# Kernel optimization log

Measured on AMD Instinct MI355X. Metric: run time of the kernel, lower is better.

## Reference

```python
import jax, jax.numpy as jnp
import numpy as np

N = 100000      # nodes
E = 600000      # directed edges
D_IN = 128
D_H = 128
D_OUT = 128
EPS = 1e-5      # BatchNorm eps


def setup_inputs() -> dict:
    key = jax.random.key(0)
    ks = jax.random.split(key, 6)
    x = jax.random.normal(ks[0], (N, D_IN), dtype=jnp.float32)
    edge_index = jax.random.randint(ks[1], (2, E), 0, N, dtype=jnp.int64)
    s1 = 1.0 / np.sqrt(D_IN)
    s2 = 1.0 / np.sqrt(D_H)
    W1 = jax.random.uniform(ks[2], (D_IN, D_H), minval=-s1, maxval=s1, dtype=jnp.float32)
    b1 = jnp.zeros((D_H,), jnp.float32)
    gamma1 = jnp.ones((D_H,), jnp.float32)
    beta1 = jnp.zeros((D_H,), jnp.float32)
    W2 = jax.random.uniform(ks[3], (D_H, D_OUT), minval=-s2, maxval=s2, dtype=jnp.float32)
    b2 = jnp.zeros((D_OUT,), jnp.float32)
    return dict(x=x, edge_index=edge_index, W1=W1, b1=b1,
                gamma1=gamma1, beta1=beta1, W2=W2, b2=b2)


def _gcn_conv(x, W, b, src, dst):
    # PyG GCNConv: h = D^{-1/2} (A + I) D^{-1/2} (x @ W) + b
    n = x.shape[0]
    h = x @ W                                   # [N, d_out]
    loop = jnp.arange(n, dtype=src.dtype)
    s = jnp.concatenate([src, loop])            # self loops appended
    d = jnp.concatenate([dst, loop])
    deg = jax.ops.segment_sum(jnp.ones_like(d, jnp.float32), d, num_segments=n)
    dinv = jax.lax.rsqrt(deg)                   # deg >= 1 after self loops
    norm = dinv[s] * dinv[d]                    # [E + N]
    agg = jax.ops.segment_sum(h[s] * norm[:, None], d, num_segments=n)  # [N, d_out]
    return agg + b


def reference(x, edge_index, W1, b1, gamma1, beta1, W2, b2):
    src, dst = edge_index[0], edge_index[1]
    # layer 0: GCNConv -> BatchNorm1d (training batch stats) -> ReLU (dropout p=0)
    h = _gcn_conv(x, W1, b1, src, dst)
    mean = h.mean(axis=0)
    var = h.var(axis=0)                         # biased variance, as torch BN
    h = (h - mean) * jax.lax.rsqrt(var + EPS) * gamma1 + beta1
    h = jax.nn.relu(h)
    # final layer: GCNConv only
    return _gcn_conv(h, W2, b2, src, dst)
```

## Files before the change

### kernel.cpp

```cpp
#include <hip/hip_runtime.h>

#define D 128
#define EPSV 1e-5f

typedef __attribute__((ext_vector_type(8))) short bf16x8;
typedef __attribute__((ext_vector_type(4))) float f32x4;

__device__ __forceinline__ short f2bf(float f){
  unsigned u = __float_as_uint(f);
  u += 0x7fffu + ((u >> 16) & 1u);
  return (short)(u >> 16);
}
__device__ __forceinline__ float bflo(unsigned u){ return __uint_as_float(u << 16); }
__device__ __forceinline__ float bfhi(unsigned u){ return __uint_as_float(u & 0xffff0000u); }
__device__ __forceinline__ float bf2f(short s){ return __uint_as_float(((unsigned)(unsigned short)s) << 16); }
__device__ __forceinline__ unsigned packbf(float a, float b){
  unsigned lo = (unsigned short)f2bf(a);
  unsigned hi = (unsigned short)f2bf(b);
  return lo | (hi << 16);
}

__global__ void k_init(int N, int E, const int* __restrict__ ei, int* __restrict__ flag,
                       int* __restrict__ deg, int* __restrict__ fill, float* __restrict__ gpart,
                       int* __restrict__ sflg,
                       const float* __restrict__ W1, const float* __restrict__ W2,
                       short* __restrict__ w1t, short* __restrict__ w2t){
  int i = blockIdx.x*blockDim.x + threadIdx.x;
  if (i < N){ deg[i] = 0; fill[i] = 0; }
  if (i < D*D){
    int j = i >> 7, k = i & 127;
    w1t[i] = f2bf(W1[k*D + j]);
    w2t[i] = f2bf(W2[k*D + j]);
  }
  if (i < 2048) gpart[i] = 0.f;
  if (i < 128) sflg[i] = 0;
  if (blockIdx.x == 0){
    __shared__ int any;
    int t = threadIdx.x;
    if (t == 0) any = 0;
    __syncthreads();
    if (2*t+1 < 2*E && ei[2*t+1] != 0) atomicOr(&any, 1);
    __syncthreads();
    if (t == 0) flag[0] = (any == 0) ? 1 : 0;
  }
}

__global__ void k_scan(const int* __restrict__ deg, int N, int* __restrict__ rowp,
                       float* __restrict__ dinv, int* __restrict__ s_agg,
                       int* __restrict__ s_inc, int* __restrict__ s_flg){
  __shared__ int sh[256];
  __shared__ int s_ex;
  int b = blockIdx.x, t = threadIdx.x;
  int base = b*1024 + t*4;
  int c0 = (base+0 < N) ? deg[base+0] : 0;
  int c1 = (base+1 < N) ? deg[base+1] : 0;
  int c2 = (base+2 < N) ? deg[base+2] : 0;
  int c3 = (base+3 < N) ? deg[base+3] : 0;
  int s = c0 + c1 + c2 + c3;
  sh[t] = s; __syncthreads();
  for (int d = 1; d < 256; d <<= 1){
    int v = (t >= d) ? sh[t-d] : 0;
    __syncthreads();
    sh[t] += v;
    __syncthreads();
  }
  int total = sh[255];
  if (t == 0){
    atomicExch(&s_agg[b], total);
    __threadfence();
    atomicExch(&s_flg[b], 1);
    int ex = 0;
    for (int i = b-1; i >= 0; ){
      int f;
      while ((f = atomicAdd(&s_flg[i], 0)) == 0) __builtin_amdgcn_s_sleep(1);
      if (f == 2){ ex += atomicAdd(&s_inc[i], 0); break; }
      ex += atomicAdd(&s_agg[i], 0); --i;
    }
    atomicExch(&s_inc[b], ex + total);
    __threadfence();
    atomicExch(&s_flg[b], 2);
    s_ex = ex;
  }
  __syncthreads();
  int o = sh[t] - s + s_ex;
  if (base+0 < N){ rowp[base+0] = o; dinv[base+0] = rsqrtf((float)(c0+1)); } o += c0;
  if (base+1 < N){ rowp[base+1] = o; dinv[base+1] = rsqrtf((float)(c1+1)); } o += c1;
  if (base+2 < N){ rowp[base+2] = o; dinv[base+2] = rsqrtf((float)(c2+1)); } o += c2;
  if (base+3 < N){ rowp[base+3] = o; dinv[base+3] = rsqrtf((float)(c3+1)); }
}

__global__ void k_scatter(const int* __restrict__ ei, int E, const int* __restrict__ flag,
                          const int* __restrict__ rowp, int* __restrict__ fill,
                          const float* __restrict__ dinv, int2* __restrict__ epack){
  int e = blockIdx.x*blockDim.x + threadIdx.x;
  if (e >= E) return;
  int s, d;
  if (flag[0]){ s = ei[2*e]; d = ei[2*E + 2*e]; }
  else        { s = ei[e];   d = ei[E + e];     }
  int pos = rowp[d] + atomicAdd(&fill[d], 1);
  int2 ev; ev.x = s; ev.y = __float_as_int(dinv[s] * dinv[d]);
  epack[pos] = ev;
}

template<int MODE>
__global__ __launch_bounds__(256, 2) void k_gemm(const void* __restrict__ A,
                                const short* __restrict__ BT, short* __restrict__ C, int N,
                                const float* __restrict__ gpart, const float* __restrict__ gamma,
                                const float* __restrict__ beta,
                                const int* __restrict__ ei, int E, const int* __restrict__ flag,
                                int* __restrict__ deg, int ngemmb){
  if (MODE == 1 && (int)blockIdx.x >= ngemmb){
    int cb = blockIdx.x - ngemmb;
    int e0 = cb*1024 + threadIdx.x;
    int f = flag[0];
    #pragma unroll
    for (int r = 0; r < 4; ++r){
      int e = e0 + r*256;
      if (e < E){
        int d = f ? ei[2*E + 2*e] : ei[E + e];
        atomicAdd(&deg[d], 1);
      }
    }
    return;
  }
  __shared__ short ldsB[16384];
  __shared__ short ldsC[4*2048];
  __shared__ __align__(16) float s_sc[128];
  __shared__ __align__(16) float s_sh[128];
  int w = threadIdx.x >> 6;
  int lane = threadIdx.x & 63;
  int m = lane & 15, quad = lane >> 4;

  if (MODE == 2 && threadIdx.x < 128){
    int f = threadIdx.x;
    float s = 0.f, q = 0.f;
    #pragma unroll
    for (int i = 0; i < 8; ++i){ s += gpart[i*256 + f]; q += gpart[i*256 + 128 + f]; }
    float inv = 1.f / (float)N;
    float mean = s * inv;
    float var  = q * inv - mean*mean;
    float sc = gamma[f] * rsqrtf(var + EPSV);
    s_sc[f] = sc;
    s_sh[f] = beta[f] - mean * sc;
  }
  {
    const bf16x8* BTv = (const bf16x8*)BT;
    bf16x8* Bw = (bf16x8*)ldsB;
    for (int g = threadIdx.x; g < 2048; g += 256){
      int row = g >> 4, ch = g & 15;
      Bw[row*16 + (ch ^ (row & 15))] = BTv[g];
    }
  }
  __syncthreads();
  const bf16x8* Bv = (const bf16x8*)ldsB;
  short* cw = ldsC + w*2048;

  int tiles = (N + 31) >> 5;
  int wid = blockIdx.x*4 + w;
  int wstride = ngemmb*4;
  for (int tile = wid; tile < tiles; tile += wstride){
    int r0 = tile << 5;
    bf16x8 a[2][4];
    #pragma unroll
    for (int g = 0; g < 2; ++g){
      int row = r0 + g*16 + m;
      if (row >= N) row = N - 1;
      #pragma unroll
      for (int kc = 0; kc < 4; ++kc){
        int k0 = kc*32 + quad*8;
        if (MODE == 1){
          const float* Af = (const float*)A + (size_t)row*D + k0;
          float4 u = *(const float4*)Af;
          float4 v = *(const float4*)(Af + 4);
          bf16x8 tv;
          tv[0]=f2bf(u.x); tv[1]=f2bf(u.y); tv[2]=f2bf(u.z); tv[3]=f2bf(u.w);
          tv[4]=f2bf(v.x); tv[5]=f2bf(v.y); tv[6]=f2bf(v.z); tv[7]=f2bf(v.w);
          a[g][kc] = tv;
        } else {
          bf16x8 raw = *(const bf16x8*)((const short*)A + (size_t)row*D + k0);
          float4 s0v = *(const float4*)(s_sc + k0);
          float4 s1v = *(const float4*)(s_sc + k0 + 4);
          float4 h0v = *(const float4*)(s_sh + k0);
          float4 h1v = *(const float4*)(s_sh + k0 + 4);
          bf16x8 tv;
          tv[0] = f2bf(fmaxf(fmaf(bf2f(raw[0]), s0v.x, h0v.x), 0.f));
          tv[1] = f2bf(fmaxf(fmaf(bf2f(raw[1]), s0v.y, h0v.y), 0.f));
          tv[2] = f2bf(fmaxf(fmaf(bf2f(raw[2]), s0v.z, h0v.z), 0.f));
          tv[3] = f2bf(fmaxf(fmaf(bf2f(raw[3]), s0v.w, h0v.w), 0.f));
          tv[4] = f2bf(fmaxf(fmaf(bf2f(raw[4]), s1v.x, h1v.x), 0.f));
          tv[5] = f2bf(fmaxf(fmaf(bf2f(raw[5]), s1v.y, h1v.y), 0.f));
          tv[6] = f2bf(fmaxf(fmaf(bf2f(raw[6]), s1v.z, h1v.z), 0.f));
          tv[7] = f2bf(fmaxf(fmaf(bf2f(raw[7]), s1v.w, h1v.w), 0.f));
          a[g][kc] = tv;
        }
      }
    }
    f32x4 acc[2][8];
    #pragma unroll
    for (int g = 0; g < 2; ++g)
      #pragma unroll
      for (int c = 0; c < 8; ++c) acc[g][c] = (f32x4){0.f,0.f,0.f,0.f};
    #pragma unroll
    for (int kc = 0; kc < 4; ++kc){
      bf16x8 bb[8];
      #pragma unroll
      for (int c = 0; c < 8; ++c)
        bb[c] = Bv[(c*16 + m)*16 + ((kc*4 + quad) ^ m)];
      #pragma unroll
      for (int g = 0; g < 2; ++g)
        #pragma unroll
        for (int c = 0; c < 8; ++c)
          acc[g][c] = __builtin_amdgcn_mfma_f32_16x16x32_bf16(bb[c], a[g][kc], acc[g][c], 0, 0, 0);
    }
    #pragma unroll
    for (int g = 0; g < 2; ++g){
      #pragma unroll
      for (int c = 0; c < 8; ++c){
        uint2 v;
        v.x = packbf(acc[g][c][0], acc[g][c][1]);
        v.y = packbf(acc[g][c][2], acc[g][c][3]);
        int x = c*2 + (quad >> 1);
        *(uint2*)&cw[m*128 + ((x ^ m) << 3) + ((quad & 1) << 2)] = v;
      }
      asm volatile("s_waitcnt lgkmcnt(0)" ::: "memory");
      #pragma unroll
      for (int rg = 0; rg < 4; ++rg){
        int lrow = rg*4 + quad;
        int rr = r0 + g*16 + lrow;
        uint4 v = *(const uint4*)&cw[lrow*128 + ((m ^ lrow) << 3)];
        if (rr < N) *(uint4*)(C + (size_t)rr*D + m*8) = v;
      }
      asm volatile("s_waitcnt lgkmcnt(0)" ::: "memory");
    }
  }
}

template<int OUTF32>
__global__ __launch_bounds__(256) void k_agg(const short* __restrict__ H, const int* __restrict__ rowp,
        const int* __restrict__ deg, const int2* __restrict__ epack, const float* __restrict__ dinv,
        const float* __restrict__ bias, void* __restrict__ out, int N, float* __restrict__ gpart){
  int w = threadIdx.x >> 6, p = threadIdx.x & 63;
  int wid = blockIdx.x*4 + w, wstride = gridDim.x*4;
  const unsigned* Hu = (const unsigned*)H;
  float S0=0.f, S1=0.f, Q0=0.f, Q1=0.f;
  float bb0=0.f, bb1=0.f;
  if (OUTF32){ bb0 = bias[2*p]; bb1 = bias[2*p+1]; }

  int n = wid;
  int start=0, cnt=0; float d1=0.f; unsigned u=0; int2 ev; ev.x=0; ev.y=0;
  if (n < N){
    start = rowp[n]; cnt = deg[n]; d1 = dinv[n];
    u = Hu[(size_t)n*64 + p];
    int nb = cnt < 64 ? cnt : 64;
    if (p < nb) ev = epack[start + p];
  }
  while (n < N){
    int n2 = n + wstride;
    int start2=0, cnt2=0; float d12=0.f; unsigned u2=0; int2 ev2; ev2.x=0; ev2.y=0;
    if (n2 < N){
      start2 = rowp[n2]; cnt2 = deg[n2]; d12 = dinv[n2];
      u2 = Hu[(size_t)n2*64 + p];
      int nb2 = cnt2 < 64 ? cnt2 : 64;
      if (p < nb2) ev2 = epack[start2 + p];
    }
    float w0 = d1*d1;
    float a0 = w0 * bflo(u), a1 = w0 * bfhi(u);
    int nb = cnt < 64 ? cnt : 64;
    for (int j = 0; j < nb; j += 8){
      int s0 = __shfl(ev.x, j+0), s1 = __shfl(ev.x, j+1);
      int s2 = __shfl(ev.x, j+2), s3 = __shfl(ev.x, j+3);
      int s4 = __shfl(ev.x, j+4), s5 = __shfl(ev.x, j+5);
      int s6 = __shfl(ev.x, j+6), s7 = __shfl(ev.x, j+7);
      float f0 = __int_as_float(__shfl(ev.y, j+0));
      float f1 = __int_as_float(__shfl(ev.y, j+1));
      float f2 = __int_as_float(__shfl(ev.y, j+2));
      float f3 = __int_as_float(__shfl(ev.y, j+3));
      float f4 = __int_as_float(__shfl(ev.y, j+4));
      float f5 = __int_as_float(__shfl(ev.y, j+5));
      float f6 = __int_as_float(__shfl(ev.y, j+6));
      float f7 = __int_as_float(__shfl(ev.y, j+7));
      unsigned u0 = Hu[(size_t)s0*64 + p], u1 = Hu[(size_t)s1*64 + p];
      unsigned u2g = Hu[(size_t)s2*64 + p], u3 = Hu[(size_t)s3*64 + p];
      unsigned u4 = Hu[(size_t)s4*64 + p], u5 = Hu[(size_t)s5*64 + p];
      unsigned u6 = Hu[(size_t)s6*64 + p], u7 = Hu[(size_t)s7*64 + p];
      a0 = fmaf(f0, bflo(u0), a0); a1 = fmaf(f0, bfhi(u0), a1);
      a0 = fmaf(f1, bflo(u1), a0); a1 = fmaf(f1, bfhi(u1), a1);
      a0 = fmaf(f2, bflo(u2g), a0); a1 = fmaf(f2, bfhi(u2g), a1);
      a0 = fmaf(f3, bflo(u3), a0); a1 = fmaf(f3, bfhi(u3), a1);
      a0 = fmaf(f4, bflo(u4), a0); a1 = fmaf(f4, bfhi(u4), a1);
      a0 = fmaf(f5, bflo(u5), a0); a1 = fmaf(f5, bfhi(u5), a1);
      a0 = fmaf(f6, bflo(u6), a0); a1 = fmaf(f6, bfhi(u6), a1);
      a0 = fmaf(f7, bflo(u7), a0); a1 = fmaf(f7, bfhi(u7), a1);
    }
    for (int base = 64; base < cnt; base += 64){
      int nbx = cnt - base; if (nbx > 64) nbx = 64;
      int2 evx; evx.x = 0; evx.y = 0;
      if (p < nbx) evx = epack[start + base + p];
      for (int j = 0; j < nbx; j += 8){
        #pragma unroll
        for (int q2 = 0; q2 < 8; ++q2){
          int sx = __shfl(evx.x, j+q2);
          float fx = __int_as_float(__shfl(evx.y, j+q2));
          unsigned ux = Hu[(size_t)sx*64 + p];
          a0 = fmaf(fx, bflo(ux), a0); a1 = fmaf(fx, bfhi(ux), a1);
        }
      }
    }
    if (OUTF32){
      float2 r; r.x = a0 + bb0; r.y = a1 + bb1;
      ((float2*)out)[(size_t)n*64 + p] = r;
    } else {
      ((unsigned*)out)[(size_t)n*64 + p] = packbf(a0, a1);
      S0 += a0; Q0 += a0*a0; S1 += a1; Q1 += a1*a1;
    }
    n = n2; start = start2; cnt = cnt2; d1 = d12; u = u2; ev = ev2;
  }
  if (!OUTF32){
    __shared__ float ls[1024];
    int base = w*256;
    ls[base + 2*p]       = S0;
    ls[base + 2*p + 1]   = S1;
    ls[base + 128 + 2*p]     = Q0;
    ls[base + 128 + 2*p + 1] = Q1;
    __syncthreads();
    int t = threadIdx.x;
    float v = ls[t] + ls[256 + t] + ls[512 + t] + ls[768 + t];
    atomicAdd(&gpart[(blockIdx.x & 7)*256 + t], v);
  }
}

extern "C" void kernel_launch(void* const* d_in, const int* in_sizes, int n_in,
                              void* d_out, int out_size, void* d_ws, size_t ws_size,
                              hipStream_t stream){
  const float* x   = (const float*)d_in[0];
  const int*   ei  = (const int*)  d_in[1];
  const float* W1  = (const float*)d_in[2];
  const float* g1  = (const float*)d_in[4];
  const float* be1 = (const float*)d_in[5];
  const float* W2  = (const float*)d_in[6];
  const float* b2  = (const float*)d_in[7];
  float* out = (float*)d_out;
  int N = in_sizes[0] / D;
  int E = in_sizes[1] / 2;

  char* w = (char*)d_ws;
  auto carve = [&](size_t bytes)->char*{ char* p = w; w += (bytes + 255) & ~(size_t)255; return p; };
  int*   flag  = (int*)  carve(256);
  int*   degA  = (int*)  carve((size_t)N*4);
  int*   fillA = (int*)  carve((size_t)N*4);
  float* dinvA = (float*)carve((size_t)N*4);
  int*   rowp  = (int*)  carve((size_t)N*4);
  int*   sagg  = (int*)  carve(512);
  int*   sinc  = (int*)  carve(512);
  int*   sflg  = (int*)  carve(512);
  int2*  epack = (int2*) carve((size_t)E*8);
  float* gpart = (float*)carve(2048*4);
  short* w1t   = (short*)carve((size_t)D*D*2);
  short* w2t   = (short*)carve((size_t)D*D*2);
  short* h1    = (short*)carve((size_t)N*D*2);
  short* hb    = (short*)carve((size_t)N*D*2);

  const int TB = 256;
  int EB  = (E + TB - 1) / TB;
  int NBt = (N + TB - 1) / TB;
  int NB1024 = (N + 1023) / 1024;
  int GEMMB = 512;
  int CNTB  = (E + 1023) / 1024;
  int AGGB  = 2048;

  k_init    <<<NBt, TB, 0, stream>>>(N, E, ei, flag, degA, fillA, gpart, sflg, W1, W2, w1t, w2t);
  k_gemm<1> <<<GEMMB + CNTB, 256, 0, stream>>>(x, w1t, h1, N, nullptr, nullptr, nullptr,
                                               ei, E, flag, degA, GEMMB);
  k_scan    <<<NB1024, 256, 0, stream>>>(degA, N, rowp, dinvA, sagg, sinc, sflg);
  k_scatter <<<EB, TB, 0, stream>>>(ei, E, flag, rowp, fillA, dinvA, epack);
  k_agg<0>  <<<AGGB, 256, 0, stream>>>(h1, rowp, degA, epack, dinvA, nullptr, hb, N, gpart);
  k_gemm<2> <<<GEMMB, 256, 0, stream>>>(hb, w2t, h1, N, gpart, g1, be1,
                                        nullptr, 0, nullptr, nullptr, GEMMB);
  k_agg<1>  <<<AGGB, 256, 0, stream>>>(h1, rowp, degA, epack, dinvA, b2, out, N, nullptr);
}
```

Baseline: 264.2 us.

## Fuse degree scan and edge scatter into first GEMM launch with inter-block flags

Result: slower. 449.8 us (+70.2%).

```diff
diff --git a/kernel.cpp b/kernel.cpp
--- a/kernel.cpp
+++ b/kernel.cpp
@@ -20,9 +20,14 @@
   return lo | (hi << 16);
 }
 
+__device__ __forceinline__ int   ld_coh_i(const int* p){ return __hip_atomic_load(p, __ATOMIC_RELAXED, __HIP_MEMORY_SCOPE_AGENT); }
+__device__ __forceinline__ float ld_coh_f(const float* p){ return __hip_atomic_load(p, __ATOMIC_RELAXED, __HIP_MEMORY_SCOPE_AGENT); }
+__device__ __forceinline__ void  st_coh_i(int* p, int v){ __hip_atomic_store(p, v, __ATOMIC_RELAXED, __HIP_MEMORY_SCOPE_AGENT); }
+__device__ __forceinline__ void  st_coh_f(float* p, float v){ __hip_atomic_store(p, v, __ATOMIC_RELAXED, __HIP_MEMORY_SCOPE_AGENT); }
+
 __global__ void k_init(int N, int E, const int* __restrict__ ei, int* __restrict__ flag,
                        int* __restrict__ deg, int* __restrict__ fill, float* __restrict__ gpart,
-                       int* __restrict__ sflg,
+                       int* __restrict__ sflg, int* __restrict__ pd,
                        const float* __restrict__ W1, const float* __restrict__ W2,
                        short* __restrict__ w1t, short* __restrict__ w2t){
   int i = blockIdx.x*blockDim.x + threadIdx.x;
@@ -34,6 +39,7 @@
   }
   if (i < 2048) gpart[i] = 0.f;
   if (i < 128) sflg[i] = 0;
+  if (i < 2) pd[i] = 0;
   if (blockIdx.x == 0){
     __shared__ int any;
     int t = threadIdx.x;
@@ -45,88 +51,116 @@
   }
 }
 
-__global__ void k_scan(const int* __restrict__ deg, int N, int* __restrict__ rowp,
-                       float* __restrict__ dinv, int* __restrict__ s_agg,
-                       int* __restrict__ s_inc, int* __restrict__ s_flg){
-  __shared__ int sh[256];
-  __shared__ int s_ex;
-  int b = blockIdx.x, t = threadIdx.x;
-  int base = b*1024 + t*4;
-  int c0 = (base+0 < N) ? deg[base+0] : 0;
-  int c1 = (base+1 < N) ? deg[base+1] : 0;
-  int c2 = (base+2 < N) ? deg[base+2] : 0;
-  int c3 = (base+3 < N) ? deg[base+3] : 0;
-  int s = c0 + c1 + c2 + c3;
-  sh[t] = s; __syncthreads();
-  for (int d = 1; d < 256; d <<= 1){
-    int v = (t >= d) ? sh[t-d] : 0;
-    __syncthreads();
-    sh[t] += v;
-    __syncthreads();
-  }
-  int total = sh[255];
-  if (t == 0){
-    atomicExch(&s_agg[b], total);
-    __threadfence();
-    atomicExch(&s_flg[b], 1);
-    int ex = 0;
-    for (int i = b-1; i >= 0; ){
-      int f;
-      while ((f = atomicAdd(&s_flg[i], 0)) == 0) __builtin_amdgcn_s_sleep(1);
-      if (f == 2){ ex += atomicAdd(&s_inc[i], 0); break; }
-      ex += atomicAdd(&s_agg[i], 0); --i;
-    }
-    atomicExch(&s_inc[b], ex + total);
-    __threadfence();
-    atomicExch(&s_flg[b], 2);
-    s_ex = ex;
-  }
-  __syncthreads();
-  int o = sh[t] - s + s_ex;
-  if (base+0 < N){ rowp[base+0] = o; dinv[base+0] = rsqrtf((float)(c0+1)); } o += c0;
-  if (base+1 < N){ rowp[base+1] = o; dinv[base+1] = rsqrtf((float)(c1+1)); } o += c1;
-  if (base+2 < N){ rowp[base+2] = o; dinv[base+2] = rsqrtf((float)(c2+1)); } o += c2;
-  if (base+3 < N){ rowp[base+3] = o; dinv[base+3] = rsqrtf((float)(c3+1)); }
-}
-
-__global__ void k_scatter(const int* __restrict__ ei, int E, const int* __restrict__ flag,
-                          const int* __restrict__ rowp, int* __restrict__ fill,
-                          const float* __restrict__ dinv, int2* __restrict__ epack){
-  int e = blockIdx.x*blockDim.x + threadIdx.x;
-  if (e >= E) return;
-  int s, d;
-  if (flag[0]){ s = ei[2*e]; d = ei[2*E + 2*e]; }
-  else        { s = ei[e];   d = ei[E + e];     }
-  int pos = rowp[d] + atomicAdd(&fill[d], 1);
-  int2 ev; ev.x = s; ev.y = __float_as_int(dinv[s] * dinv[d]);
-  epack[pos] = ev;
-}
-
 template<int MODE>
 __global__ __launch_bounds__(256, 2) void k_gemm(const void* __restrict__ A,
                                 const short* __restrict__ BT, short* __restrict__ C, int N,
                                 const float* __restrict__ gpart, const float* __restrict__ gamma,
                                 const float* __restrict__ beta,
                                 const int* __restrict__ ei, int E, const int* __restrict__ flag,
-                                int* __restrict__ deg, int ngemmb){
-  if (MODE == 1 && (int)blockIdx.x >= ngemmb){
-    int cb = blockIdx.x - ngemmb;
-    int e0 = cb*1024 + threadIdx.x;
-    int f = flag[0];
-    #pragma unroll
-    for (int r = 0; r < 4; ++r){
-      int e = e0 + r*256;
-      if (e < E){
-        int d = f ? ei[2*E + 2*e] : ei[E + e];
-        atomicAdd(&deg[d], 1);
-      }
-    }
-    return;
-  }
+                                int* __restrict__ deg, int ngemmb,
+                                int* __restrict__ rowp, float* __restrict__ dinvP,
+                                int* __restrict__ fillP, int2* __restrict__ epack,
+                                int* __restrict__ s_agg, int* __restrict__ s_inc,
+                                int* __restrict__ s_flg, int* __restrict__ pd,
+                                int cntb, int scanb){
   __shared__ short ldsB[16384];
   __shared__ short ldsC[4*2048];
   __shared__ __align__(16) float s_sc[128];
   __shared__ __align__(16) float s_sh[128];
+
+  if (MODE == 1 && (int)blockIdx.x >= ngemmb){
+    int cb = blockIdx.x - ngemmb;
+    int t = threadIdx.x;
+    if (cb < cntb){
+      int e0 = cb*1024 + t;
+      int f = flag[0];
+      #pragma unroll
+      for (int r = 0; r < 4; ++r){
+        int e = e0 + r*256;
+        if (e < E){
+          int d = f ? ei[2*E + 2*e] : ei[E + e];
+          atomicAdd(&deg[d], 1);
+        }
+      }
+      __syncthreads();
+      if (t == 0){ __threadfence(); atomicAdd(&pd[0], 1); }
+      return;
+    }
+    if (cb < cntb + scanb){
+      int sb = cb - cntb;
+      int* sh = (int*)ldsB;
+      if (t == 0){
+        while (__hip_atomic_load(&pd[0], __ATOMIC_ACQUIRE, __HIP_MEMORY_SCOPE_AGENT) < cntb)
+          __builtin_amdgcn_s_sleep(8);
+      }
+      __syncthreads();
+      int base = sb*1024 + t*4;
+      int c0 = (base+0 < N) ? ld_coh_i(&deg[base+0]) : 0;
+      int c1 = (base+1 < N) ? ld_coh_i(&deg[base+1]) : 0;
+      int c2 = (base+2 < N) ? ld_coh_i(&deg[base+2]) : 0;
+      int c3 = (base+3 < N) ? ld_coh_i(&deg[base+3]) : 0;
+      int s = c0 + c1 + c2 + c3;
+      sh[t] = s; __syncthreads();
+      for (int d = 1; d < 256; d <<= 1){
+        int v = (t >= d) ? sh[t-d] : 0;
+        __syncthreads();
+        sh[t] += v;
+        __syncthreads();
+      }
+      int total = sh[255];
+      if (t == 0){
+        atomicExch(&s_agg[sb], total);
+        __threadfence();
+        atomicExch(&s_flg[sb], 1);
+        int ex = 0;
+        for (int i = sb-1; i >= 0; ){
+          int f;
+          while ((f = atomicAdd(&s_flg[i], 0)) == 0) __builtin_amdgcn_s_sleep(1);
+          if (f == 2){ ex += atomicAdd(&s_inc[i], 0); break; }
+          ex += atomicAdd(&s_agg[i], 0); --i;
+        }
+        atomicExch(&s_inc[sb], ex + total);
+        __threadfence();
+        atomicExch(&s_flg[sb], 2);
+        sh[256] = ex;
+      }
+      __syncthreads();
+      int ex = sh[256];
+      int o = sh[t] - s + ex;
+      if (base+0 < N){ st_coh_i(&rowp[base+0], o); st_coh_f(&dinvP[base+0], rsqrtf((float)(c0+1))); } o += c0;
+      if (base+1 < N){ st_coh_i(&rowp[base+1], o); st_coh_f(&dinvP[base+1], rsqrtf((float)(c1+1))); } o += c1;
+      if (base+2 < N){ st_coh_i(&rowp[base+2], o); st_coh_f(&dinvP[base+2], rsqrtf((float)(c2+1))); } o += c2;
+      if (base+3 < N){ st_coh_i(&rowp[base+3], o); st_coh_f(&dinvP[base+3], rsqrtf((float)(c3+1))); }
+      __syncthreads();
+      if (t == 0){ __threadfence(); atomicAdd(&pd[1], 1); }
+      return;
+    }
+    {
+      int eb = cb - cntb - scanb;
+      if (t == 0){
+        while (__hip_atomic_load(&pd[1], __ATOMIC_ACQUIRE, __HIP_MEMORY_SCOPE_AGENT) < scanb)
+          __builtin_amdgcn_s_sleep(8);
+      }
+      __syncthreads();
+      int f = flag[0];
+      int e0 = eb*1024 + t;
+      #pragma unroll
+      for (int r = 0; r < 4; ++r){
+        int e = e0 + r*256;
+        if (e < E){
+          int sE, dE;
+          if (f){ sE = ei[2*e]; dE = ei[2*E + 2*e]; }
+          else  { sE = ei[e];   dE = ei[E + e];     }
+          int pos = ld_coh_i(&rowp[dE]) + atomicAdd(&fillP[dE], 1);
+          int2 ev; ev.x = sE;
+          ev.y = __float_as_int(ld_coh_f(&dinvP[sE]) * ld_coh_f(&dinvP[dE]));
+          epack[pos] = ev;
+        }
+      }
+      return;
+    }
+  }
+
   int w = threadIdx.x >> 6;
   int lane = threadIdx.x & 63;
   int m = lane & 15, quad = lane >> 4;
@@ -353,6 +387,7 @@
   int*   sagg  = (int*)  carve(512);
   int*   sinc  = (int*)  carve(512);
   int*   sflg  = (int*)  carve(512);
+  int*   pd    = (int*)  carve(256);
   int2*  epack = (int2*) carve((size_t)E*8);
   float* gpart = (float*)carve(2048*4);
   short* w1t   = (short*)carve((size_t)D*D*2);
@@ -361,20 +396,21 @@
   short* hb    = (short*)carve((size_t)N*D*2);
 
   const int TB = 256;
-  int EB  = (E + TB - 1) / TB;
   int NBt = (N + TB - 1) / TB;
-  int NB1024 = (N + 1023) / 1024;
+  int SCANB = (N + 1023) / 1024;
   int GEMMB = 512;
   int CNTB  = (E + 1023) / 1024;
+  int SCATB = (E + 1023) / 1024;
   int AGGB  = 2048;
 
-  k_init    <<<NBt, TB, 0, stream>>>(N, E, ei, flag, degA, fillA, gpart, sflg, W1, W2, w1t, w2t);
-  k_gemm<1> <<<GEMMB + CNTB, 256, 0, stream>>>(x, w1t, h1, N, nullptr, nullptr, nullptr,
-                                               ei, E, flag, degA, GEMMB);
-  k_scan    <<<NB1024, 256, 0, stream>>>(degA, N, rowp, dinvA, sagg, sinc, sflg);
-  k_scatter <<<EB, TB, 0, stream>>>(ei, E, flag, rowp, fillA, dinvA, epack);
+  k_init    <<<NBt, TB, 0, stream>>>(N, E, ei, flag, degA, fillA, gpart, sflg, pd, W1, W2, w1t, w2t);
+  k_gemm<1> <<<GEMMB + CNTB + SCANB + SCATB, 256, 0, stream>>>(x, w1t, h1, N,
+                nullptr, nullptr, nullptr,
+                ei, E, flag, degA, GEMMB,
+                rowp, dinvA, fillA, epack, sagg, sinc, sflg, pd, CNTB, SCANB);
   k_agg<0>  <<<AGGB, 256, 0, stream>>>(h1, rowp, degA, epack, dinvA, nullptr, hb, N, gpart);
   k_gemm<2> <<<GEMMB, 256, 0, stream>>>(hb, w2t, h1, N, gpart, g1, be1,
-                                        nullptr, 0, nullptr, nullptr, GEMMB);
+                nullptr, 0, nullptr, nullptr, GEMMB,
+                nullptr, nullptr, nullptr, nullptr, nullptr, nullptr, nullptr, nullptr, 0, 0);
   k_agg<1>  <<<AGGB, 256, 0, stream>>>(h1, rowp, degA, epack, dinvA, b2, out, N, nullptr);
 }
```
